# Kernel optimization log

Hardware: AMD Instinct MI355X
Metric: run time of the kernel (lower is better)

The kernel has to match this reference:

```python
import jax, jax.numpy as jnp
import numpy as np

N_NODES = 50000
N_EDGES = 300000
IN_CH = 128
HIDDEN = 64
OUT_CH = 40
NUM_LAYERS = 4
HEADS = 8


def setup_inputs() -> dict:
    key = jax.random.key(0)
    ks = jax.random.split(key, 8)
    s = lambda fan_in: 1.0 / np.sqrt(fan_in)
    return {
        "x": jax.random.normal(ks[0], (N_NODES, IN_CH), dtype=jnp.float32),
        "edge_index": jax.random.randint(ks[1], (2, N_EDGES), 0, N_NODES, dtype=jnp.int64),
        "heads": HEADS,
        "w1": jax.random.uniform(ks[2], (IN_CH, HIDDEN), jnp.float32, -s(IN_CH), s(IN_CH)),
        "b1": jnp.zeros((HIDDEN,), jnp.float32),
        "wq": jax.random.uniform(ks[3], (NUM_LAYERS, HIDDEN, HIDDEN), jnp.float32, -s(HIDDEN), s(HIDDEN)),
        "wk": jax.random.uniform(ks[4], (NUM_LAYERS, HIDDEN, HIDDEN), jnp.float32, -s(HIDDEN), s(HIDDEN)),
        "wv": jax.random.uniform(ks[5], (NUM_LAYERS, HIDDEN, HIDDEN), jnp.float32, -s(HIDDEN), s(HIDDEN)),
        "w2": jax.random.uniform(ks[6], (HIDDEN, OUT_CH), jnp.float32, -s(HIDDEN), s(HIDDEN)),
        "b2": jnp.zeros((OUT_CH,), jnp.float32),
    }


def _dna_conv(x_all, src, dst, norm, wq, wk, wv, heads):
    # x_all: [N, L, C]; attention of each node's latest state over neighbors' full history.
    N, L, C = x_all.shape
    d = C // heads
    q = (x_all[:, -1] @ wq).reshape(N, heads, d)      # [N, h, d]
    k = (x_all @ wk).reshape(N, L, heads, d)          # [N, L, h, d]
    v = (x_all @ wv).reshape(N, L, heads, d)
    qe = q[dst]                                       # [E, h, d]
    ke = k[src]                                       # [E, L, h, d]
    ve = v[src]
    scale = 1.0 / jnp.sqrt(jnp.asarray(d, x_all.dtype))
    score = jnp.einsum('ehd,elhd->ehl', qe, ke) * scale
    attn = jax.nn.softmax(score, axis=-1)             # softmax over history L
    msg = jnp.einsum('ehl,elhd->ehd', attn, ve).reshape(-1, C)
    msg = msg * norm[:, None]                         # GCN symmetric norm per edge
    return jax.ops.segment_sum(msg, dst, num_segments=N)  # sum-aggregate at target


def reference(x, edge_index, heads, w1, b1, wq, wk, wv, w2, b2):
    N = x.shape[0]
    loop = jnp.arange(N, dtype=edge_index.dtype)
    src = jnp.concatenate([edge_index[0], loop])      # gcn_norm adds self loops
    dst = jnp.concatenate([edge_index[1], loop])
    ew = jnp.ones(src.shape[0], x.dtype)
    deg = jax.ops.segment_sum(ew, dst, num_segments=N)
    dinv = jnp.where(deg > 0, jax.lax.rsqrt(deg), 0.0)
    norm = dinv[src] * dinv[dst]

    h = jax.nn.relu(x @ w1 + b1)                      # lin1 + ReLU (DFALayer = identity fwd)
    x_all = h[:, None, :]                             # [N, 1, C]
    for i in range(wq.shape[0]):
        out = jax.nn.relu(_dna_conv(x_all, src, dst, norm, wq[i], wk[i], wv[i], heads))
        x_all = jnp.concatenate([x_all, out[:, None, :]], axis=1)
    logits = x_all[:, -1] @ w2 + b2
    return jax.nn.log_softmax(logits, axis=1)
```

## Files before the change

kernel.cpp:

```cpp
#include <hip/hip_runtime.h>
#include <hip/hip_fp16.h>
#include <math.h>

#define N_NODES 50000
#define N_EDGES 300000
#define E_TOT (N_EDGES + N_NODES)
#define IN_CH 128
#define HIDDEN 64
#define OUT_CH 40
#define NUM_LAYERS 4
#define NCHUNK ((N_NODES + 255) / 256)
#define NTILES (N_NODES / 16)
#define QKV_WPR 512

typedef _Float16 h8 __attribute__((ext_vector_type(8)));
typedef float f32x4 __attribute__((ext_vector_type(4)));

#define MFMA16(a, b, c) __builtin_amdgcn_mfma_f32_16x16x32_f16((a), (b), (c), 0, 0, 0)

__global__ void k_count_init(int* count, int* fill) {
    int n = blockIdx.x * blockDim.x + threadIdx.x;
    if (n < N_NODES) { count[n] = 1; fill[n] = 1; }
}

__global__ void k_count(const int* __restrict__ dst, int* count) {
    int e = blockIdx.x * blockDim.x + threadIdx.x;
    if (e < N_EDGES) atomicAdd(&count[dst[e]], 1);
}

__global__ __launch_bounds__(256) void k_scan_a(const int* __restrict__ count,
                                                int* __restrict__ loc,
                                                int* __restrict__ psum) {
    __shared__ int s[256];
    int tid = threadIdx.x;
    int g = blockIdx.x * 256 + tid;
    int v = (g < N_NODES) ? count[g] : 0;
    s[tid] = v;
    __syncthreads();
    for (int off = 1; off < 256; off <<= 1) {
        int t = (tid >= off) ? s[tid - off] : 0;
        __syncthreads();
        s[tid] += t;
        __syncthreads();
    }
    if (g < N_NODES) loc[g] = s[tid] - v;
    if (tid == 255) psum[blockIdx.x] = s[255];
}

__global__ __launch_bounds__(256) void k_scan_b(int* psum) {
    __shared__ int s[256];
    int tid = threadIdx.x;
    int v = (tid < NCHUNK) ? psum[tid] : 0;
    s[tid] = v;
    __syncthreads();
    for (int off = 1; off < 256; off <<= 1) {
        int t = (tid >= off) ? s[tid - off] : 0;
        __syncthreads();
        s[tid] += t;
        __syncthreads();
    }
    if (tid < NCHUNK) psum[tid] = s[tid] - v;
}

__global__ void k_scan_c(const int* __restrict__ count, const int* __restrict__ loc,
                         const int* __restrict__ psum, int* __restrict__ rowptr,
                         float* __restrict__ dinv, int* __restrict__ ssrc,
                         float* __restrict__ snorm) {
    int n = blockIdx.x * blockDim.x + threadIdx.x;
    if (n >= N_NODES) return;
    int rp = loc[n] + psum[n >> 8];
    rowptr[n] = rp;
    float di = rsqrtf((float)count[n]);
    dinv[n] = di;
    ssrc[rp] = n;
    snorm[rp] = di * di;
    if (n == 0) rowptr[N_NODES] = E_TOT;
}

__global__ void k_scatter(const int* __restrict__ ei, const int* __restrict__ rowptr,
                          int* __restrict__ fill, const float* __restrict__ dinv,
                          int* __restrict__ ssrc, float* __restrict__ snorm) {
    int e = blockIdx.x * blockDim.x + threadIdx.x;
    if (e >= N_EDGES) return;
    int s = ei[e], d = ei[N_EDGES + e];
    int p = rowptr[d] + atomicAdd(&fill[d], 1);
    ssrc[p] = s;
    snorm[p] = dinv[s] * dinv[d];
}

__device__ __forceinline__ h8 load_bfrag(const float* __restrict__ W, int ncols,
                                         int kbase, int c) {
    h8 r;
#pragma unroll
    for (int i = 0; i < 8; ++i) r[i] = (_Float16)W[(kbase + i) * ncols + c];
    return r;
}

__global__ __launch_bounds__(256) void k_h_mfma(const float* __restrict__ x,
                                                const float* __restrict__ w1,
                                                const float* __restrict__ b1,
                                                float* __restrict__ xall,
                                                __half* __restrict__ xh) {
    int lane = threadIdx.x & 63;
    int gw = blockIdx.x * 4 + (threadIdx.x >> 6);
    int krow = lane >> 4, col = lane & 15;
    h8 B[4][4];
#pragma unroll
    for (int ct = 0; ct < 4; ++ct)
#pragma unroll
        for (int s = 0; s < 4; ++s)
            B[ct][s] = load_bfrag(w1, HIDDEN, krow * 8 + 32 * s, ct * 16 + col);
    float bias[4];
#pragma unroll
    for (int ct = 0; ct < 4; ++ct) bias[ct] = b1[ct * 16 + col];
    for (int t = gw; t < NTILES; t += 1024) {
        int n0 = t * 16;
        const float* xrow = x + (size_t)(n0 + col) * IN_CH + krow * 8;
        f32x4 acc[4] = {{0.f, 0.f, 0.f, 0.f}, {0.f, 0.f, 0.f, 0.f},
                        {0.f, 0.f, 0.f, 0.f}, {0.f, 0.f, 0.f, 0.f}};
#pragma unroll
        for (int s = 0; s < 4; ++s) {
            float4 p0 = *(const float4*)(xrow + 32 * s);
            float4 p1 = *(const float4*)(xrow + 32 * s + 4);
            h8 a;
            a[0] = (_Float16)p0.x; a[1] = (_Float16)p0.y;
            a[2] = (_Float16)p0.z; a[3] = (_Float16)p0.w;
            a[4] = (_Float16)p1.x; a[5] = (_Float16)p1.y;
            a[6] = (_Float16)p1.z; a[7] = (_Float16)p1.w;
#pragma unroll
            for (int ct = 0; ct < 4; ++ct) acc[ct] = MFMA16(a, B[ct][s], acc[ct]);
        }
#pragma unroll
        for (int ct = 0; ct < 4; ++ct)
#pragma unroll
            for (int reg = 0; reg < 4; ++reg) {
                float v = fmaxf(acc[ct][reg] + bias[ct], 0.f);
                size_t o = (size_t)(n0 + krow * 4 + reg) * 320 + ct * 16 + col;
                xall[o] = v;
                xh[o] = __float2half(v);
            }
    }
}

template <int L>
__global__ __launch_bounds__(256) void k_qkv_mfma(const __half* __restrict__ xh,
                                                  const float* __restrict__ wq,
                                                  const float* __restrict__ wk,
                                                  const float* __restrict__ wv,
                                                  __half* __restrict__ qh,
                                                  __half* __restrict__ kh,
                                                  __half* __restrict__ vh) {
    int lane = threadIdx.x & 63;
    int gw = blockIdx.x * 4 + (threadIdx.x >> 6);
    int role = gw / QKV_WPR;
    int slot = gw - role * QKV_WPR;
    int krow = lane >> 4, col = lane & 15;
    if (role == 0) {
        int lx = L - 1;
        h8 B[4][2];
#pragma unroll
        for (int ct = 0; ct < 4; ++ct)
#pragma unroll
            for (int s = 0; s < 2; ++s)
                B[ct][s] = load_bfrag(wq, HIDDEN, krow * 8 + 32 * s, ct * 16 + col);
        for (int t = slot; t < NTILES; t += QKV_WPR) {
            int n0 = t * 16;
            const __half* ap = xh + (size_t)(n0 + col) * 320 + lx * 64 + krow * 8;
            h8 a0 = *(const h8*)(const void*)ap;
            h8 a1 = *(const h8*)(const void*)(ap + 32);
            f32x4 acc[4] = {{0.f, 0.f, 0.f, 0.f}, {0.f, 0.f, 0.f, 0.f},
                            {0.f, 0.f, 0.f, 0.f}, {0.f, 0.f, 0.f, 0.f}};
#pragma unroll
            for (int ct = 0; ct < 4; ++ct) {
                acc[ct] = MFMA16(a0, B[ct][0], acc[ct]);
                acc[ct] = MFMA16(a1, B[ct][1], acc[ct]);
            }
#pragma unroll
            for (int ct = 0; ct < 4; ++ct)
#pragma unroll
                for (int reg = 0; reg < 4; ++reg)
                    qh[(size_t)(n0 + krow * 4 + reg) * 64 + ct * 16 + col] =
                        __float2half(acc[ct][reg] * 0.35355339059327373f);
        }
    } else {
        int lx = role - 1;
        h8 Bk[4][2], Bv[4][2];
#pragma unroll
        for (int ct = 0; ct < 4; ++ct)
#pragma unroll
            for (int s = 0; s < 2; ++s) {
                Bk[ct][s] = load_bfrag(wk, HIDDEN, krow * 8 + 32 * s, ct * 16 + col);
                Bv[ct][s] = load_bfrag(wv, HIDDEN, krow * 8 + 32 * s, ct * 16 + col);
            }
        for (int t = slot; t < NTILES; t += QKV_WPR) {
            int n0 = t * 16;
            const __half* ap = xh + (size_t)(n0 + col) * 320 + lx * 64 + krow * 8;
            h8 a0 = *(const h8*)(const void*)ap;
            h8 a1 = *(const h8*)(const void*)(ap + 32);
            f32x4 ak[4] = {{0.f, 0.f, 0.f, 0.f}, {0.f, 0.f, 0.f, 0.f},
                           {0.f, 0.f, 0.f, 0.f}, {0.f, 0.f, 0.f, 0.f}};
            f32x4 av[4] = {{0.f, 0.f, 0.f, 0.f}, {0.f, 0.f, 0.f, 0.f},
                           {0.f, 0.f, 0.f, 0.f}, {0.f, 0.f, 0.f, 0.f}};
#pragma unroll
            for (int ct = 0; ct < 4; ++ct) {
                ak[ct] = MFMA16(a0, Bk[ct][0], ak[ct]);
                ak[ct] = MFMA16(a1, Bk[ct][1], ak[ct]);
                av[ct] = MFMA16(a0, Bv[ct][0], av[ct]);
                av[ct] = MFMA16(a1, Bv[ct][1], av[ct]);
            }
#pragma unroll
            for (int ct = 0; ct < 4; ++ct)
#pragma unroll
                for (int reg = 0; reg < 4; ++reg) {
                    size_t o = (size_t)(n0 + krow * 4 + reg) * (L * 64) + lx * 64 +
                               ct * 16 + col;
                    kh[o] = __float2half(ak[ct][reg]);
                    vh[o] = __float2half(av[ct][reg]);
                }
        }
    }
}

template <int L>
__global__ __launch_bounds__(256) void k_edge_csr8(const int* __restrict__ rowptr,
                                                   const int* __restrict__ ssrc,
                                                   const float* __restrict__ snorm,
                                                   const __half* __restrict__ kh,
                                                   const __half* __restrict__ vh,
                                                   const __half* __restrict__ qh,
                                                   float* __restrict__ xall,
                                                   __half* __restrict__ xh) {
    int tid = threadIdx.x;
    int wid = tid >> 6, lane = tid & 63;
    int g = lane >> 3, r = lane & 7;
    int d = blockIdx.x * 4 + wid;
    if (d >= N_NODES) return;
    int rs = rowptr[d], re = rowptr[d + 1];
    float qf[8];
    {
        float4 raw = ((const float4*)(qh + (size_t)d * 64))[r];
        const __half2* hp = (const __half2*)&raw;
#pragma unroll
        for (int i = 0; i < 4; ++i) {
            float2 f = __half22float2(hp[i]);
            qf[2 * i] = f.x; qf[2 * i + 1] = f.y;
        }
    }
    float acc[8];
#pragma unroll
    for (int i = 0; i < 8; ++i) acc[i] = 0.f;
    for (int base = rs; base < re; base += 8) {
        int eidx = base + g;
        bool valid = eidx < re;
        int s = valid ? ssrc[eidx] : 0;
        float nrm = valid ? snorm[eidx] : 0.f;
        float sc[L];
        float4 vraw[L];
#pragma unroll
        for (int l = 0; l < L; ++l) {
            size_t rowo = ((size_t)s * L + l) * 64 + r * 8;
            float4 kraw = *(const float4*)(kh + rowo);
            vraw[l] = *(const float4*)(vh + rowo);
            const __half2* hp = (const __half2*)&kraw;
            float p = 0.f;
#pragma unroll
            for (int i = 0; i < 4; ++i) {
                float2 f = __half22float2(hp[i]);
                p = fmaf(qf[2 * i], f.x, p);
                p = fmaf(qf[2 * i + 1], f.y, p);
            }
            sc[l] = p;
        }
        float m = sc[0];
#pragma unroll
        for (int l = 1; l < L; ++l) m = fmaxf(m, sc[l]);
        float ssum = 0.f;
#pragma unroll
        for (int l = 0; l < L; ++l) { sc[l] = __expf(sc[l] - m); ssum += sc[l]; }
        float w = __fdividef(nrm, ssum);
#pragma unroll
        for (int l = 0; l < L; ++l) {
            float swl = sc[l] * w;
            const __half2* hp = (const __half2*)&vraw[l];
#pragma unroll
            for (int i = 0; i < 4; ++i) {
                float2 f = __half22float2(hp[i]);
                acc[2 * i] = fmaf(swl, f.x, acc[2 * i]);
                acc[2 * i + 1] = fmaf(swl, f.y, acc[2 * i + 1]);
            }
        }
    }
#pragma unroll
    for (int i = 0; i < 8; ++i) {
        acc[i] += __shfl_xor(acc[i], 8);
        acc[i] += __shfl_xor(acc[i], 16);
        acc[i] += __shfl_xor(acc[i], 32);
    }
    if (lane < 8) {
        float4 o0, o1;
        o0.x = fmaxf(acc[0], 0.f); o0.y = fmaxf(acc[1], 0.f);
        o0.z = fmaxf(acc[2], 0.f); o0.w = fmaxf(acc[3], 0.f);
        o1.x = fmaxf(acc[4], 0.f); o1.y = fmaxf(acc[5], 0.f);
        o1.z = fmaxf(acc[6], 0.f); o1.w = fmaxf(acc[7], 0.f);
        float4* op = (float4*)(xall + (size_t)d * 320 + L * 64);
        op[r * 2] = o0; op[r * 2 + 1] = o1;
        __half hbuf[8];
        hbuf[0] = __float2half(o0.x); hbuf[1] = __float2half(o0.y);
        hbuf[2] = __float2half(o0.z); hbuf[3] = __float2half(o0.w);
        hbuf[4] = __float2half(o1.x); hbuf[5] = __float2half(o1.y);
        hbuf[6] = __float2half(o1.z); hbuf[7] = __float2half(o1.w);
        *(float4*)(xh + (size_t)d * 320 + L * 64 + r * 8) = *(float4*)hbuf;
    }
}

__global__ __launch_bounds__(256) void k_final_lds(const float* __restrict__ xall,
                                                   const float* __restrict__ w2,
                                                   const float* __restrict__ b2,
                                                   float* __restrict__ out) {
    __shared__ float rows[16][HIDDEN];
    int tid = threadIdx.x, wid = tid >> 6, lane = tid & 63;
    int cl = (lane < OUT_CH) ? lane : (OUT_CH - 1);
    float wcol[HIDDEN];
#pragma unroll
    for (int j = 0; j < HIDDEN; ++j) wcol[j] = w2[j * OUT_CH + cl];
    float b = b2[cl];
    for (int t = blockIdx.x; t < NTILES; t += gridDim.x) {
        int n0 = t * 16;
        {
            int rr = tid >> 4, seg = tid & 15;
            *(float4*)&rows[rr][seg * 4] =
                *(const float4*)&xall[(size_t)(n0 + rr) * 320 + 256 + seg * 4];
        }
        __syncthreads();
#pragma unroll
        for (int u = 0; u < 4; ++u) {
            int ln = wid * 4 + u;
            const float4* rp = (const float4*)rows[ln];
            float a0 = 0.f, a1 = 0.f, a2 = 0.f, a3 = 0.f;
#pragma unroll
            for (int jc = 0; jc < HIDDEN / 4; ++jc) {
                float4 r = rp[jc];
                a0 = fmaf(r.x, wcol[jc * 4 + 0], a0);
                a1 = fmaf(r.y, wcol[jc * 4 + 1], a1);
                a2 = fmaf(r.z, wcol[jc * 4 + 2], a2);
                a3 = fmaf(r.w, wcol[jc * 4 + 3], a3);
            }
            float logit = (lane < OUT_CH) ? ((a0 + a1) + (a2 + a3) + b) : -INFINITY;
            float m = logit;
            for (int mask = 32; mask; mask >>= 1) m = fmaxf(m, __shfl_xor(m, mask));
            float ex = (lane < OUT_CH) ? __expf(logit - m) : 0.f;
            float ssum = ex;
            for (int mask = 32; mask; mask >>= 1) ssum += __shfl_xor(ssum, mask);
            if (lane < OUT_CH)
                out[(size_t)(n0 + ln) * OUT_CH + lane] = logit - m - logf(ssum);
        }
        __syncthreads();
    }
}

extern "C" void kernel_launch(void* const* d_in, const int* in_sizes, int n_in,
                              void* d_out, int out_size, void* d_ws, size_t ws_size,
                              hipStream_t stream) {
    const float* x  = (const float*)d_in[0];
    const int*   ei = (const int*)d_in[1];
    const float* w1 = (const float*)d_in[3];
    const float* b1 = (const float*)d_in[4];
    const float* wq = (const float*)d_in[5];
    const float* wk = (const float*)d_in[6];
    const float* wv = (const float*)d_in[7];
    const float* w2 = (const float*)d_in[8];
    const float* b2 = (const float*)d_in[9];
    float* out = (float*)d_out;

    char* cur = (char*)d_ws;
    auto alloc = [&](size_t bytes) { char* p = cur; cur += (bytes + 255) & ~(size_t)255; return p; };
    float*   dinv   = (float*)alloc(N_NODES * 4);
    float*   xall   = (float*)alloc((size_t)N_NODES * 320 * 4);
    __half*  xh     = (__half*)alloc((size_t)N_NODES * 320 * 2);
    __half*  qh     = (__half*)alloc((size_t)N_NODES * 64 * 2);
    __half*  kh     = (__half*)alloc((size_t)N_NODES * 256 * 2);
    __half*  vh     = (__half*)alloc((size_t)N_NODES * 256 * 2);
    int*     count  = (int*)alloc(N_NODES * 4);
    int*     loc    = (int*)alloc(N_NODES * 4);
    int*     psum   = (int*)alloc(256 * 4);
    int*     rowptr = (int*)alloc((N_NODES + 1) * 4);
    int*     fill   = (int*)alloc(N_NODES * 4);
    int*     ssrc   = (int*)alloc((size_t)E_TOT * 4);
    float*   snorm  = (float*)alloc((size_t)E_TOT * 4);

    k_count_init<<<(N_NODES + 255) / 256, 256, 0, stream>>>(count, fill);
    k_count<<<(N_EDGES + 255) / 256, 256, 0, stream>>>(ei + N_EDGES, count);
    k_scan_a<<<NCHUNK, 256, 0, stream>>>(count, loc, psum);
    k_scan_b<<<1, 256, 0, stream>>>(psum);
    k_scan_c<<<(N_NODES + 255) / 256, 256, 0, stream>>>(count, loc, psum, rowptr,
                                                        dinv, ssrc, snorm);
    k_scatter<<<(N_EDGES + 255) / 256, 256, 0, stream>>>(ei, rowptr, fill, dinv,
                                                         ssrc, snorm);

    k_h_mfma<<<256, 256, 0, stream>>>(x, w1, b1, xall, xh);

    for (int i = 0; i < NUM_LAYERS; ++i) {
        int L = i + 1;
        int qkvblk = (L + 1) * (QKV_WPR / 4);
        const float* wqi = wq + i * 4096;
        const float* wki = wk + i * 4096;
        const float* wvi = wv + i * 4096;
        switch (L) {
            case 1:
                k_qkv_mfma<1><<<qkvblk, 256, 0, stream>>>(xh, wqi, wki, wvi, qh, kh, vh);
                k_edge_csr8<1><<<(N_NODES + 3) / 4, 256, 0, stream>>>(rowptr, ssrc, snorm, kh, vh, qh, xall, xh);
                break;
            case 2:
                k_qkv_mfma<2><<<qkvblk, 256, 0, stream>>>(xh, wqi, wki, wvi, qh, kh, vh);
                k_edge_csr8<2><<<(N_NODES + 3) / 4, 256, 0, stream>>>(rowptr, ssrc, snorm, kh, vh, qh, xall, xh);
                break;
            case 3:
                k_qkv_mfma<3><<<qkvblk, 256, 0, stream>>>(xh, wqi, wki, wvi, qh, kh, vh);
                k_edge_csr8<3><<<(N_NODES + 3) / 4, 256, 0, stream>>>(rowptr, ssrc, snorm, kh, vh, qh, xall, xh);
                break;
            default:
                k_qkv_mfma<4><<<qkvblk, 256, 0, stream>>>(xh, wqi, wki, wvi, qh, kh, vh);
                k_edge_csr8<4><<<(N_NODES + 3) / 4, 256, 0, stream>>>(rowptr, ssrc, snorm, kh, vh, qh, xall, xh);
                break;
        }
    }
    k_final_lds<<<512, 256, 0, stream>>>(xall, w2, b2, out);
}
```

Measured before the change: 301.1 us.

## Specialize layer one, use head-major interleaved K/V layout, drop fp32 history

Layer 1 has a single history entry, so the softmax weight is 1; the code now computes only V for it and aggregates without Q/K work. Later layers store K and V interleaved in a head-major layout, so each block handles one head and gathers contiguous 16-half chunks per source node. Lanes are split across history slots and a cross-lane shuffle computes the softmax. The fp32 full-history buffer is removed, and only the last layer writes fp32 output for the final linear. The head-per-block split re-reads rowptr, ssrc and snorm eight times, and the grid-stride loop adds scheduling overhead.

```diff
diff --git a/kernel.cpp b/kernel.cpp
--- a/kernel.cpp
+++ b/kernel.cpp
@@ -12,6 +12,7 @@
 #define NCHUNK ((N_NODES + 255) / 256)
 #define NTILES (N_NODES / 16)
 #define QKV_WPR 512
+#define EDGE_SLOTS 2048
 
 typedef _Float16 h8 __attribute__((ext_vector_type(8)));
 typedef float f32x4 __attribute__((ext_vector_type(4)));
@@ -96,10 +97,19 @@
     return r;
 }
 
+__device__ __forceinline__ void unpack8(float4 raw, float* f) {
+    const __half2* hp = (const __half2*)&raw;
+#pragma unroll
+    for (int i = 0; i < 4; ++i) {
+        float2 t = __half22float2(hp[i]);
+        f[2 * i] = t.x;
+        f[2 * i + 1] = t.y;
+    }
+}
+
 __global__ __launch_bounds__(256) void k_h_mfma(const float* __restrict__ x,
                                                 const float* __restrict__ w1,
                                                 const float* __restrict__ b1,
-                                                float* __restrict__ xall,
                                                 __half* __restrict__ xh) {
     int lane = threadIdx.x & 63;
     int gw = blockIdx.x * 4 + (threadIdx.x >> 6);
@@ -135,10 +145,80 @@
 #pragma unroll
             for (int reg = 0; reg < 4; ++reg) {
                 float v = fmaxf(acc[ct][reg] + bias[ct], 0.f);
-                size_t o = (size_t)(n0 + krow * 4 + reg) * 320 + ct * 16 + col;
-                xall[o] = v;
-                xh[o] = __float2half(v);
-            }
+                xh[(size_t)(n0 + krow * 4 + reg) * 320 + ct * 16 + col] = __float2half(v);
+            }
+    }
+}
+
+__global__ __launch_bounds__(256) void k_v1_mfma(const __half* __restrict__ xh,
+                                                 const float* __restrict__ wv,
+                                                 __half* __restrict__ vh1) {
+    int lane = threadIdx.x & 63;
+    int gw = blockIdx.x * 4 + (threadIdx.x >> 6);
+    int krow = lane >> 4, col = lane & 15;
+    h8 B[4][2];
+#pragma unroll
+    for (int ct = 0; ct < 4; ++ct)
+#pragma unroll
+        for (int s = 0; s < 2; ++s)
+            B[ct][s] = load_bfrag(wv, HIDDEN, krow * 8 + 32 * s, ct * 16 + col);
+    for (int t = gw; t < NTILES; t += QKV_WPR) {
+        int n0 = t * 16;
+        const __half* ap = xh + (size_t)(n0 + col) * 320 + krow * 8;
+        h8 a0 = *(const h8*)(const void*)ap;
+        h8 a1 = *(const h8*)(const void*)(ap + 32);
+        f32x4 acc[4] = {{0.f, 0.f, 0.f, 0.f}, {0.f, 0.f, 0.f, 0.f},
+                        {0.f, 0.f, 0.f, 0.f}, {0.f, 0.f, 0.f, 0.f}};
+#pragma unroll
+        for (int ct = 0; ct < 4; ++ct) {
+            acc[ct] = MFMA16(a0, B[ct][0], acc[ct]);
+            acc[ct] = MFMA16(a1, B[ct][1], acc[ct]);
+        }
+#pragma unroll
+        for (int ct = 0; ct < 4; ++ct)
+#pragma unroll
+            for (int reg = 0; reg < 4; ++reg)
+                vh1[(size_t)(n0 + krow * 4 + reg) * 64 + ct * 16 + col] =
+                    __float2half(acc[ct][reg]);
+    }
+}
+
+__global__ __launch_bounds__(256) void k_edge_l1(const int* __restrict__ rowptr,
+                                                 const int* __restrict__ ssrc,
+                                                 const float* __restrict__ snorm,
+                                                 const __half* __restrict__ vh1,
+                                                 __half* __restrict__ xh) {
+    int tid = threadIdx.x;
+    int wid = tid >> 6, lane = tid & 63;
+    int g = lane >> 3, r = lane & 7;
+    int d = blockIdx.x * 4 + wid;
+    if (d >= N_NODES) return;
+    int rs = rowptr[d], re = rowptr[d + 1];
+    float acc[8];
+#pragma unroll
+    for (int i = 0; i < 8; ++i) acc[i] = 0.f;
+    for (int base = rs; base < re; base += 8) {
+        int eidx = base + g;
+        bool valid = eidx < re;
+        int s = valid ? ssrc[eidx] : 0;
+        float nrm = valid ? snorm[eidx] : 0.f;
+        float4 raw = *(const float4*)(vh1 + (size_t)s * 64 + r * 8);
+        float f[8];
+        unpack8(raw, f);
+#pragma unroll
+        for (int c = 0; c < 8; ++c) acc[c] = fmaf(nrm, f[c], acc[c]);
+    }
+#pragma unroll
+    for (int c = 0; c < 8; ++c) {
+        acc[c] += __shfl_xor(acc[c], 8);
+        acc[c] += __shfl_xor(acc[c], 16);
+        acc[c] += __shfl_xor(acc[c], 32);
+    }
+    if (lane < 8) {
+        __half hbuf[8];
+#pragma unroll
+        for (int c = 0; c < 8; ++c) hbuf[c] = __float2half(fmaxf(acc[c], 0.f));
+        *(float4*)(xh + (size_t)d * 320 + 64 + r * 8) = *(float4*)hbuf;
     }
 }
 
@@ -148,8 +228,7 @@
                                                   const float* __restrict__ wk,
                                                   const float* __restrict__ wv,
                                                   __half* __restrict__ qh,
-                                                  __half* __restrict__ kh,
-                                                  __half* __restrict__ vh) {
+                                                  __half* __restrict__ kvh) {
     int lane = threadIdx.x & 63;
     int gw = blockIdx.x * 4 + (threadIdx.x >> 6);
     int role = gw / QKV_WPR;
@@ -212,108 +291,104 @@
             for (int ct = 0; ct < 4; ++ct)
 #pragma unroll
                 for (int reg = 0; reg < 4; ++reg) {
-                    size_t o = (size_t)(n0 + krow * 4 + reg) * (L * 64) + lx * 64 +
-                               ct * 16 + col;
-                    kh[o] = __float2half(ak[ct][reg]);
-                    vh[o] = __float2half(av[ct][reg]);
+                    int n = n0 + krow * 4 + reg;
+                    int ch = ct * 16 + col;
+                    int h = ch >> 3, c = ch & 7;
+                    size_t base = (((size_t)h * N_NODES + n) * L + lx) * 16 + c;
+                    kvh[base] = __float2half(ak[ct][reg]);
+                    kvh[base + 8] = __float2half(av[ct][reg]);
                 }
         }
     }
 }
 
 template <int L>
-__global__ __launch_bounds__(256) void k_edge_csr8(const int* __restrict__ rowptr,
-                                                   const int* __restrict__ ssrc,
-                                                   const float* __restrict__ snorm,
-                                                   const __half* __restrict__ kh,
-                                                   const __half* __restrict__ vh,
-                                                   const __half* __restrict__ qh,
-                                                   float* __restrict__ xall,
-                                                   __half* __restrict__ xh) {
+__global__ __launch_bounds__(256) void k_edge_hm(const int* __restrict__ rowptr,
+                                                 const int* __restrict__ ssrc,
+                                                 const float* __restrict__ snorm,
+                                                 const __half* __restrict__ kvh,
+                                                 const __half* __restrict__ qh,
+                                                 float* __restrict__ aggout,
+                                                 __half* __restrict__ xh) {
+    constexpr int S = (L == 2) ? 4 : 8;
+    constexpr int E = 64 / S;
     int tid = threadIdx.x;
     int wid = tid >> 6, lane = tid & 63;
-    int g = lane >> 3, r = lane & 7;
-    int d = blockIdx.x * 4 + wid;
-    if (d >= N_NODES) return;
-    int rs = rowptr[d], re = rowptr[d + 1];
-    float qf[8];
-    {
-        float4 raw = ((const float4*)(qh + (size_t)d * 64))[r];
-        const __half2* hp = (const __half2*)&raw;
-#pragma unroll
-        for (int i = 0; i < 4; ++i) {
-            float2 f = __half22float2(hp[i]);
-            qf[2 * i] = f.x; qf[2 * i + 1] = f.y;
-        }
-    }
-    float acc[8];
-#pragma unroll
-    for (int i = 0; i < 8; ++i) acc[i] = 0.f;
-    for (int base = rs; base < re; base += 8) {
-        int eidx = base + g;
-        bool valid = eidx < re;
-        int s = valid ? ssrc[eidx] : 0;
-        float nrm = valid ? snorm[eidx] : 0.f;
-        float sc[L];
-        float4 vraw[L];
-#pragma unroll
-        for (int l = 0; l < L; ++l) {
-            size_t rowo = ((size_t)s * L + l) * 64 + r * 8;
-            float4 kraw = *(const float4*)(kh + rowo);
-            vraw[l] = *(const float4*)(vh + rowo);
-            const __half2* hp = (const __half2*)&kraw;
+    int h = blockIdx.x & 7;
+    int slot = blockIdx.x >> 3;
+    int g = lane / S, sub = lane & (S - 1);
+    int l = sub >> 1, j = sub & 1;
+    int lc = (l < L) ? l : (L - 1);
+    int sgbase = lane & ~(S - 1);
+    for (int d = slot * 4 + wid; d < N_NODES; d += EDGE_SLOTS * 4) {
+        int rs = rowptr[d], re = rowptr[d + 1];
+        float qf[8];
+        unpack8(*(const float4*)(qh + (size_t)d * 64 + h * 8), qf);
+        float acc[8];
+#pragma unroll
+        for (int c = 0; c < 8; ++c) acc[c] = 0.f;
+        for (int base = rs; base < re; base += E) {
+            int eidx = base + g;
+            bool valid = eidx < re;
+            int s = valid ? ssrc[eidx] : 0;
+            float nrm = valid ? snorm[eidx] : 0.f;
+            float4 raw = *(const float4*)(
+                kvh + ((((size_t)h * N_NODES + s) * L + lc) * 2 + j) * 8);
+            float f[8];
+            unpack8(raw, f);
             float p = 0.f;
 #pragma unroll
-            for (int i = 0; i < 4; ++i) {
-                float2 f = __half22float2(hp[i]);
-                p = fmaf(qf[2 * i], f.x, p);
-                p = fmaf(qf[2 * i + 1], f.y, p);
-            }
-            sc[l] = p;
-        }
-        float m = sc[0];
-#pragma unroll
-        for (int l = 1; l < L; ++l) m = fmaxf(m, sc[l]);
-        float ssum = 0.f;
-#pragma unroll
-        for (int l = 0; l < L; ++l) { sc[l] = __expf(sc[l] - m); ssum += sc[l]; }
-        float w = __fdividef(nrm, ssum);
-#pragma unroll
-        for (int l = 0; l < L; ++l) {
-            float swl = sc[l] * w;
-            const __half2* hp = (const __half2*)&vraw[l];
-#pragma unroll
-            for (int i = 0; i < 4; ++i) {
-                float2 f = __half22float2(hp[i]);
-                acc[2 * i] = fmaf(swl, f.x, acc[2 * i]);
-                acc[2 * i + 1] = fmaf(swl, f.y, acc[2 * i + 1]);
-            }
-        }
-    }
-#pragma unroll
-    for (int i = 0; i < 8; ++i) {
-        acc[i] += __shfl_xor(acc[i], 8);
-        acc[i] += __shfl_xor(acc[i], 16);
-        acc[i] += __shfl_xor(acc[i], 32);
-    }
-    if (lane < 8) {
-        float4 o0, o1;
-        o0.x = fmaxf(acc[0], 0.f); o0.y = fmaxf(acc[1], 0.f);
-        o0.z = fmaxf(acc[2], 0.f); o0.w = fmaxf(acc[3], 0.f);
-        o1.x = fmaxf(acc[4], 0.f); o1.y = fmaxf(acc[5], 0.f);
-        o1.z = fmaxf(acc[6], 0.f); o1.w = fmaxf(acc[7], 0.f);
-        float4* op = (float4*)(xall + (size_t)d * 320 + L * 64);
-        op[r * 2] = o0; op[r * 2 + 1] = o1;
-        __half hbuf[8];
-        hbuf[0] = __float2half(o0.x); hbuf[1] = __float2half(o0.y);
-        hbuf[2] = __float2half(o0.z); hbuf[3] = __float2half(o0.w);
-        hbuf[4] = __float2half(o1.x); hbuf[5] = __float2half(o1.y);
-        hbuf[6] = __float2half(o1.z); hbuf[7] = __float2half(o1.w);
-        *(float4*)(xh + (size_t)d * 320 + L * 64 + r * 8) = *(float4*)hbuf;
-    }
-}
-
-__global__ __launch_bounds__(256) void k_final_lds(const float* __restrict__ xall,
+            for (int c = 0; c < 8; ++c) p = fmaf(qf[c], f[c], p);
+            float sc[L];
+            float m = -1e30f;
+#pragma unroll
+            for (int ll = 0; ll < L; ++ll) {
+                sc[ll] = __shfl(p, sgbase + 2 * ll, 64);
+                m = fmaxf(m, sc[ll]);
+            }
+            float ssum = 0.f;
+#pragma unroll
+            for (int ll = 0; ll < L; ++ll) {
+                sc[ll] = __expf(sc[ll] - m);
+                ssum += sc[ll];
+            }
+            float w = __fdividef(nrm, ssum);
+            float my_e = 0.f;
+#pragma unroll
+            for (int ll = 0; ll < L; ++ll) my_e = (l == ll) ? sc[ll] : my_e;
+            float a = (j == 1 && l < L) ? my_e * w : 0.f;
+#pragma unroll
+            for (int c = 0; c < 8; ++c) acc[c] = fmaf(a, f[c], acc[c]);
+        }
+#pragma unroll
+        for (int c = 0; c < 8; ++c) {
+            acc[c] += __shfl_xor(acc[c], 1);
+            acc[c] += __shfl_xor(acc[c], 2);
+            acc[c] += __shfl_xor(acc[c], 4);
+            acc[c] += __shfl_xor(acc[c], 8);
+            acc[c] += __shfl_xor(acc[c], 16);
+            acc[c] += __shfl_xor(acc[c], 32);
+        }
+        if (lane == 0) {
+            if (L == NUM_LAYERS) {
+                float4 o0, o1;
+                o0.x = fmaxf(acc[0], 0.f); o0.y = fmaxf(acc[1], 0.f);
+                o0.z = fmaxf(acc[2], 0.f); o0.w = fmaxf(acc[3], 0.f);
+                o1.x = fmaxf(acc[4], 0.f); o1.y = fmaxf(acc[5], 0.f);
+                o1.z = fmaxf(acc[6], 0.f); o1.w = fmaxf(acc[7], 0.f);
+                float4* op = (float4*)(aggout + (size_t)d * 64 + h * 8);
+                op[0] = o0; op[1] = o1;
+            } else {
+                __half hbuf[8];
+#pragma unroll
+                for (int c = 0; c < 8; ++c) hbuf[c] = __float2half(fmaxf(acc[c], 0.f));
+                *(float4*)(xh + (size_t)d * 320 + L * 64 + h * 8) = *(float4*)hbuf;
+            }
+        }
+    }
+}
+
+__global__ __launch_bounds__(256) void k_final_lds(const float* __restrict__ aggout,
                                                    const float* __restrict__ w2,
                                                    const float* __restrict__ b2,
                                                    float* __restrict__ out) {
@@ -329,7 +404,7 @@
         {
             int rr = tid >> 4, seg = tid & 15;
             *(float4*)&rows[rr][seg * 4] =
-                *(const float4*)&xall[(size_t)(n0 + rr) * 320 + 256 + seg * 4];
+                *(const float4*)&aggout[(size_t)(n0 + rr) * 64 + seg * 4];
         }
         __syncthreads();
 #pragma unroll
@@ -375,11 +450,11 @@
     char* cur = (char*)d_ws;
     auto alloc = [&](size_t bytes) { char* p = cur; cur += (bytes + 255) & ~(size_t)255; return p; };
     float*   dinv   = (float*)alloc(N_NODES * 4);
-    float*   xall   = (float*)alloc((size_t)N_NODES * 320 * 4);
     __half*  xh     = (__half*)alloc((size_t)N_NODES * 320 * 2);
+    float*   aggout = (float*)alloc((size_t)N_NODES * 64 * 4);
     __half*  qh     = (__half*)alloc((size_t)N_NODES * 64 * 2);
-    __half*  kh     = (__half*)alloc((size_t)N_NODES * 256 * 2);
-    __half*  vh     = (__half*)alloc((size_t)N_NODES * 256 * 2);
+    __half*  kvh    = (__half*)alloc((size_t)8 * N_NODES * NUM_LAYERS * 16 * 2);
+    __half*  vh1    = (__half*)alloc((size_t)N_NODES * 64 * 2);
     int*     count  = (int*)alloc(N_NODES * 4);
     int*     loc    = (int*)alloc(N_NODES * 4);
     int*     psum   = (int*)alloc(256 * 4);
@@ -397,32 +472,31 @@
     k_scatter<<<(N_EDGES + 255) / 256, 256, 0, stream>>>(ei, rowptr, fill, dinv,
                                                          ssrc, snorm);
 
-    k_h_mfma<<<256, 256, 0, stream>>>(x, w1, b1, xall, xh);
-
-    for (int i = 0; i < NUM_LAYERS; ++i) {
+    k_h_mfma<<<256, 256, 0, stream>>>(x, w1, b1, xh);
+
+    k_v1_mfma<<<QKV_WPR / 4, 256, 0, stream>>>(xh, wv, vh1);
+    k_edge_l1<<<(N_NODES + 3) / 4, 256, 0, stream>>>(rowptr, ssrc, snorm, vh1, xh);
+
+    for (int i = 1; i < NUM_LAYERS; ++i) {
         int L = i + 1;
         int qkvblk = (L + 1) * (QKV_WPR / 4);
         const float* wqi = wq + i * 4096;
         const float* wki = wk + i * 4096;
         const float* wvi = wv + i * 4096;
         switch (L) {
-            case 1:
-                k_qkv_mfma<1><<<qkvblk, 256, 0, stream>>>(xh, wqi, wki, wvi, qh, kh, vh);
-                k_edge_csr8<1><<<(N_NODES + 3) / 4, 256, 0, stream>>>(rowptr, ssrc, snorm, kh, vh, qh, xall, xh);
-                break;
             case 2:
-                k_qkv_mfma<2><<<qkvblk, 256, 0, stream>>>(xh, wqi, wki, wvi, qh, kh, vh);
-                k_edge_csr8<2><<<(N_NODES + 3) / 4, 256, 0, stream>>>(rowptr, ssrc, snorm, kh, vh, qh, xall, xh);
+                k_qkv_mfma<2><<<qkvblk, 256, 0, stream>>>(xh, wqi, wki, wvi, qh, kvh);
+                k_edge_hm<2><<<8 * EDGE_SLOTS, 256, 0, stream>>>(rowptr, ssrc, snorm, kvh, qh, aggout, xh);
                 break;
             case 3:
-                k_qkv_mfma<3><<<qkvblk, 256, 0, stream>>>(xh, wqi, wki, wvi, qh, kh, vh);
-                k_edge_csr8<3><<<(N_NODES + 3) / 4, 256, 0, stream>>>(rowptr, ssrc, snorm, kh, vh, qh, xall, xh);
+                k_qkv_mfma<3><<<qkvblk, 256, 0, stream>>>(xh, wqi, wki, wvi, qh, kvh);
+                k_edge_hm<3><<<8 * EDGE_SLOTS, 256, 0, stream>>>(rowptr, ssrc, snorm, kvh, qh, aggout, xh);
                 break;
             default:
-                k_qkv_mfma<4><<<qkvblk, 256, 0, stream>>>(xh, wqi, wki, wvi, qh, kh, vh);
-                k_edge_csr8<4><<<(N_NODES + 3) / 4, 256, 0, stream>>>(rowptr, ssrc, snorm, kh, vh, qh, xall, xh);
+                k_qkv_mfma<4><<<qkvblk, 256, 0, stream>>>(xh, wqi, wki, wvi, qh, kvh);
+                k_edge_hm<4><<<8 * EDGE_SLOTS, 256, 0, stream>>>(rowptr, ssrc, snorm, kvh, qh, aggout, xh);
                 break;
         }
     }
-    k_final_lds<<<512, 256, 0, stream>>>(xall, w2, b2, out);
-}
+    k_final_lds<<<512, 256, 0, stream>>>(aggout, w2, b2, out);
+}
```

Measured after the change: 815.7 us. 171% more time.
